# Kernel optimization log

Measured on AMD Instinct MI355X. Metric: run time of the kernel, lower is better.

## Reference

```python
import jax, jax.numpy as jnp
import numpy as np

N_HEAD, D_MODEL, DQ, DK, DV = 16, 1024, 64, 64, 64
B, LQ, LK = 2, 2048, 2048
EPS = 1e-3


def setup_inputs() -> dict:
    key = jax.random.key(0)
    ks = jax.random.split(key, 8)
    v = jax.random.normal(ks[0], (B, LK, D_MODEL), jnp.float32)
    k = jax.random.normal(ks[1], (B, LK, D_MODEL), jnp.float32)
    q = jax.random.normal(ks[2], (B, LQ, D_MODEL), jnp.float32)
    mask = jax.random.randint(ks[3], (B, LQ, LK), 0, 2).astype(bool)
    # xavier_normal for [n_head, d_model, d*]: fan_in=d_model, fan_out=d* (per torch, last two dims)
    def xav(kk, shape):
        std = np.sqrt(2.0 / (shape[-2] + shape[-1]))
        return jax.random.normal(kk, shape, jnp.float32) * std
    w_q = xav(ks[4], (N_HEAD, D_MODEL, DQ))
    w_k = xav(ks[5], (N_HEAD, D_MODEL, DK))
    w_v = xav(ks[6], (N_HEAD, D_MODEL, DV))
    # output linear: torch default init; use uniform(-1/sqrt(fan_in), ..)
    fan_in = N_HEAD * DV
    bound = 1.0 / np.sqrt(fan_in)
    kw, kb = jax.random.split(ks[7])
    w_o = jax.random.uniform(kw, (fan_in, D_MODEL), jnp.float32, -bound, bound)
    b_o = jax.random.uniform(kb, (D_MODEL,), jnp.float32, -bound, bound)
    gamma = jnp.ones((D_MODEL,), jnp.float32)
    beta = jnp.zeros((D_MODEL,), jnp.float32)
    return {"v": v, "k": k, "q": q, "mask": mask, "w_q": w_q, "w_k": w_k,
            "w_v": w_v, "w_o": w_o, "b_o": b_o, "gamma": gamma, "beta": beta}


def _layer_norm(x, gamma, beta):
    mean = jnp.mean(x, axis=-1, keepdims=True)
    # torch.std default is unbiased (ddof=1); eps added to std (not var)
    std = jnp.std(x, axis=-1, keepdims=True, ddof=1)
    return (x - mean) / (std + EPS) * gamma + beta


def reference(v, k, q, mask, w_q, w_k, w_v, w_o, b_o, gamma, beta):
    residual = k  # source uses k as residual
    # per-head projections: [h, b, l, d*]
    qh = jnp.einsum('bld,hde->hble', q, w_q)
    kh = jnp.einsum('bld,hde->hble', k, w_k)
    vh = jnp.einsum('bld,hde->hble', v, w_v)
    scale = 1.0 / np.sqrt(DK)
    scores = jnp.einsum('hbqe,hbke->hbqk', qh, kh) * scale  # [h,b,Lq,Lk]
    scores = jnp.where(mask[None], -jnp.inf, scores)
    attn = jax.nn.softmax(scores, axis=-1)
    out = jnp.einsum('hbqk,hbke->hbqe', attn, vh)  # [h,b,Lq,dv]
    # cat(split(out, batch, dim=0), dim=-1): heads concatenated on last dim
    out = out.transpose(1, 2, 0, 3).reshape(out.shape[1], out.shape[2], -1)
    out = out @ w_o + b_o
    x = out + residual  # dropout is identity in eval
    return _layer_norm(x, gamma, beta)
```

## Files before the change

### kernel.cpp

```cpp
#include <hip/hip_runtime.h>
#include <math.h>

typedef __bf16 bf16_t;
typedef bf16_t bf16x8 __attribute__((ext_vector_type(8)));
typedef float  f32x4  __attribute__((ext_vector_type(4)));
typedef unsigned short u16;
typedef u16 ushortx4 __attribute__((ext_vector_type(4)));
typedef unsigned long long u64;

#define MFMA16(a, b, c) __builtin_amdgcn_mfma_f32_16x16x32_bf16((a), (b), (c), 0, 0, 0)

__device__ __forceinline__ u16 f2bf(float f) {
    unsigned int u = __float_as_uint(f);
    u = (u + 0x7fffu + ((u >> 16) & 1u)) >> 16;
    return (u16)u;
}

__device__ __forceinline__ float bf2f(unsigned int u) {
    return __uint_as_float(u << 16);
}

__device__ __forceinline__ void gld16(const u16* g, u16* l) {
    __builtin_amdgcn_global_load_lds(
        (const __attribute__((address_space(1))) void*)g,
        (__attribute__((address_space(3))) void*)l, 16, 0, 0);
}


__global__ __launch_bounds__(256) void k_prep(const float* __restrict__ q,
                                              const float* __restrict__ k,
                                              const float* __restrict__ v,
                                              const int* __restrict__ mask,
                                              u16* __restrict__ qb,
                                              u16* __restrict__ kb,
                                              u16* __restrict__ vb,
                                              u64* __restrict__ mask64) {
    int bid = blockIdx.x;
    if (bid < 12288) {
        int sel = bid >> 12;
        int i = (bid & 4095) * 256 + threadIdx.x;
        const float* src = sel == 0 ? q : (sel == 1 ? k : v);
        u16* dst = sel == 0 ? qb : (sel == 1 ? kb : vb);
        float4 val = ((const float4*)src)[i];
        ushortx4 r;
        r[0] = f2bf(val.x); r[1] = f2bf(val.y); r[2] = f2bf(val.z); r[3] = f2bf(val.w);
        ((ushortx4*)dst)[i] = r;
    } else {
        int b2 = bid - 12288;
        int ktg = b2 & 7, q4 = (b2 >> 3) & 511, b = b2 >> 12;
        int wave = threadIdx.x >> 6, lane = threadIdx.x & 63;
        int qq = q4 * 4 + wave;
        const int* mp = mask + ((size_t)(b * 2048 + qq)) * 2048 + ktg * 256 + lane;
#pragma unroll
        for (int i = 0; i < 4; ++i) {
            int m = mp[i * 64];
            u64 bal = __ballot(m != 0);
            if (lane == 0) mask64[((size_t)(b * 32 + ktg * 4 + i)) * 2048 + qq] = bal;
        }
    }
}

__global__ __launch_bounds__(256) void k_prepw(const float* __restrict__ w_q,
                                               const float* __restrict__ w_k,
                                               const float* __restrict__ w_v,
                                               const float* __restrict__ w_o,
                                               u16* __restrict__ wqt,
                                               u16* __restrict__ wkt,
                                               u16* __restrict__ wvt,
                                               u16* __restrict__ wot) {
    __shared__ float tile[32][33];
    int bid = blockIdx.x;
    const float* src;
    u16* dst;
    int r0, c0, R, C;
    if (bid < 3072) {
        int x = bid & 31, y = (bid >> 5) & 1, z = bid >> 6;
        int h = z & 15, sel = z >> 4;
        src = (sel == 0 ? w_q : (sel == 1 ? w_k : w_v)) + (size_t)h * 65536;
        dst = (sel == 0 ? wqt : (sel == 1 ? wkt : wvt)) + (size_t)h * 65536;
        r0 = x * 32; c0 = y * 32; R = 1024; C = 64;
    } else {
        int t = bid - 3072;
        r0 = (t & 31) * 32; c0 = (t >> 5) * 32; R = 1024; C = 1024;
        src = w_o; dst = wot;
    }
    int tx = threadIdx.x & 31, ty = threadIdx.x >> 5;
    const float* s = src + ((size_t)r0) * C + c0;
#pragma unroll
    for (int i = 0; i < 4; ++i) tile[ty + i * 8][tx] = s[(ty + i * 8) * (size_t)C + tx];
    __syncthreads();
    u16* d = dst + ((size_t)c0) * R + r0;
#pragma unroll
    for (int i = 0; i < 4; ++i) d[(ty + i * 8) * (size_t)R + tx] = f2bf(tile[tx][ty + i * 8]);
}

#define GEMM_CORE(Ablk, Bblk, ACC)                                                    \
    int c0 = wave * 2;                                                                \
    const u16* Ag0 = Ablk + (size_t)(c0 * 16 + l15) * 1024 + quad * 8;                \
    const u16* Ag1 = Ablk + (size_t)((c0 + 1) * 16 + l15) * 1024 + quad * 8;          \
    const u16* Bg0 = Bblk + (size_t)(c0 * 16 + l15) * 1024 + quad * 8;                \
    const u16* Bg1 = Bblk + (size_t)((c0 + 1) * 16 + l15) * 1024 + quad * 8;          \
    gld16(Ag0, As + c0 * 512); gld16(Ag1, As + (c0 + 1) * 512);                       \
    gld16(Bg0, Bs + c0 * 512); gld16(Bg1, Bs + (c0 + 1) * 512);                       \
    __syncthreads();                                                                  \
    int buf = 0;                                                                      \
    for (int ks = 0; ks < 32; ++ks) {                                                 \
        if (ks < 31) {                                                                \
            int k0 = (ks + 1) * 32;                                                   \
            gld16(Ag0 + k0, As + (buf ^ 1) * 4096 + c0 * 512);                        \
            gld16(Ag1 + k0, As + (buf ^ 1) * 4096 + (c0 + 1) * 512);                  \
            gld16(Bg0 + k0, Bs + (buf ^ 1) * 4096 + c0 * 512);                        \
            gld16(Bg1 + k0, Bs + (buf ^ 1) * 4096 + (c0 + 1) * 512);                  \
        }                                                                             \
        bf16x8 af[4], bfr[4];                                                         \
        _Pragma("unroll")                                                             \
        for (int i = 0; i < 4; ++i)                                                   \
            af[i] = *(const bf16x8*)(As + buf * 4096 + (wy * 4 + i) * 512 + lane * 8);\
        _Pragma("unroll")                                                             \
        for (int j = 0; j < 4; ++j)                                                   \
            bfr[j] = *(const bf16x8*)(Bs + buf * 4096 + (wx * 4 + j) * 512 + lane * 8);\
        _Pragma("unroll")                                                             \
        for (int i = 0; i < 4; ++i)                                                   \
            _Pragma("unroll")                                                         \
            for (int j = 0; j < 4; ++j) ACC[i][j] = MFMA16(af[i], bfr[j], ACC[i][j]); \
        __syncthreads();                                                              \
        buf ^= 1;                                                                     \
    }

__global__ __launch_bounds__(256) void k_proj(
    const u16* __restrict__ qb, const u16* __restrict__ kb, const u16* __restrict__ vb,
    const u16* __restrict__ wqt, const u16* __restrict__ wkt, const u16* __restrict__ wvt,
    u16* __restrict__ oq, u16* __restrict__ okh, u16* __restrict__ ovt) {
    __shared__ __align__(16) u16 smem[18432];
    u16* As = smem;
    u16* Bs = smem + 8192;
    int z = blockIdx.y, gx = blockIdx.x;
    int bm, bn;
    const u16 *A, *B;
    if (z == 0)      { bm = gx >> 3; bn = gx & 7; A = qb; B = wqt; }
    else if (z == 1) { bm = gx >> 3; bn = gx & 7; A = kb; B = wkt; }
    else             { bm = gx & 7; bn = gx >> 3; A = wvt; B = vb; }
    A += (size_t)bm * 128 * 1024;
    B += (size_t)bn * 128 * 1024;
    int tid = threadIdx.x, wave = tid >> 6, lane = tid & 63;
    int wy = wave >> 1, wx = wave & 1, l15 = lane & 15, quad = lane >> 4;
    f32x4 acc[4][4] = {};
    GEMM_CORE(A, B, acc)
    u16* ep = smem + wave * 4608;
    float mulf = (z == 0) ? 0.18033688011112042f : 1.0f;
#pragma unroll
    for (int i = 0; i < 4; ++i)
#pragma unroll
        for (int j = 0; j < 4; ++j)
#pragma unroll
            for (int r = 0; r < 4; ++r)
                ep[(i * 16 + quad * 4 + r) * 72 + j * 16 + l15] = f2bf(acc[i][j][r] * mulf);
    int rl = lane >> 3, cg = lane & 7;
    if (z < 2) {
        int hh = bn * 2 + wx;
        int m0 = bm * 128 + wy * 64;
        int bb = m0 >> 11, l0 = m0 & 2047;
        u16* O = (z ? okh : oq) + ((size_t)((hh * 2 + bb) * 2048 + l0)) * 64;
#pragma unroll
        for (int s = 0; s < 8; ++s) {
            int row = s * 8 + rl;
            uint4 v = *(const uint4*)(ep + row * 72 + cg * 8);
            *(uint4*)(O + (size_t)row * 64 + cg * 8) = v;
        }
    } else {
        int m0 = bm * 128 + wy * 64;
        int hh = m0 >> 6;
        int n0 = bn * 128 + wx * 64;
        int bb = n0 >> 11, l0 = n0 & 2047;
        u16* O = ovt + (size_t)(hh * 2 + bb) * 131072 + (size_t)(m0 & 63) * 2048 + l0;
#pragma unroll
        for (int s = 0; s < 8; ++s) {
            int row = s * 8 + rl;
            uint4 v = *(const uint4*)(ep + row * 72 + cg * 8);
            *(uint4*)(O + (size_t)row * 2048 + cg * 8) = v;
        }
    }
}

__global__ __launch_bounds__(256) void k_attn(
    const u16* __restrict__ qh, const u16* __restrict__ kh,
    const u16* __restrict__ vt, const u64* __restrict__ mask64,
    u16* __restrict__ po, float* __restrict__ pl) {
    int qt = blockIdx.x, hb = blockIdx.y, ksp = blockIdx.z;
    int b = hb & 1;
    int tid = threadIdx.x, wave = tid >> 6, lane = tid & 63;
    int l15 = lane & 15, quad = lane >> 4;

    __shared__ __align__(16) u16 Ks[2][4096], Vs[2][4096];
    __shared__ __align__(16) u16 Pb[4][1024];

    int qrow0 = qt * 128 + wave * 32;
    const u16* Qp = qh + ((size_t)(hb * 2048) + qrow0 + l15) * 64 + quad * 8;
    bf16x8 qf[2][2];
    qf[0][0] = *(const bf16x8*)Qp;
    qf[0][1] = *(const bf16x8*)(Qp + 32);
    qf[1][0] = *(const bf16x8*)(Qp + 1024);
    qf[1][1] = *(const bf16x8*)(Qp + 1024 + 32);

    int c0 = wave * 2;
    const u16* Kg0 = kh + (size_t)hb * 131072 + (size_t)ksp * 65536 +
                     (size_t)(wave * 16 + l15) * 64 + quad * 8;
    const u16* Kg1 = Kg0 + 32;
    const u16* Vg0 = vt + (size_t)hb * 131072 + (size_t)(wave * 16 + l15) * 2048 +
                     ksp * 1024 + quad * 8;
    const u16* Vg1 = Vg0 + 32;
    const u64* Mp = mask64 + (size_t)b * 65536 + (size_t)ksp * 32768 + qrow0 + l15;

    float l_lane[2] = {0.f, 0.f};
    f32x4 o[2][4] = {};

    gld16(Kg0, &Ks[0][c0 * 512]);
    gld16(Kg1, &Ks[0][(c0 + 1) * 512]);
    gld16(Vg0, &Vs[0][c0 * 512]);
    gld16(Vg1, &Vs[0][(c0 + 1) * 512]);
    u64 mw0 = Mp[0], mw1 = Mp[16];
    __syncthreads();
    int buf = 0;
    int swz = (l15 & 7) << 3;
    for (int kt = 0; kt < 16; ++kt) {
        u64 mwn0 = 0, mwn1 = 0;
        if (kt < 15) {
            gld16(Kg0 + (size_t)(kt + 1) * 4096, &Ks[buf ^ 1][c0 * 512]);
            gld16(Kg1 + (size_t)(kt + 1) * 4096, &Ks[buf ^ 1][(c0 + 1) * 512]);
            gld16(Vg0 + (size_t)(kt + 1) * 64, &Vs[buf ^ 1][c0 * 512]);
            gld16(Vg1 + (size_t)(kt + 1) * 64, &Vs[buf ^ 1][(c0 + 1) * 512]);
            mwn0 = Mp[(size_t)(kt + 1) * 2048];
            mwn1 = Mp[(size_t)(kt + 1) * 2048 + 16];
        }
        bf16x8 kf[8], vf[8];
#pragma unroll
        for (int c = 0; c < 8; ++c) kf[c] = *(const bf16x8*)&Ks[buf][c * 512 + lane * 8];
#pragma unroll
        for (int c = 0; c < 8; ++c) vf[c] = *(const bf16x8*)&Vs[buf][c * 512 + lane * 8];
#pragma unroll
        for (int hf = 0; hf < 2; ++hf) {
            u64 mw = hf ? mw1 : mw0;
            f32x4 st[4] = {};
#pragma unroll
            for (int t = 0; t < 4; ++t) {
                st[t] = MFMA16(kf[t * 2], qf[hf][0], st[t]);
                st[t] = MFMA16(kf[t * 2 + 1], qf[hf][1], st[t]);
            }
            unsigned int w0 = (unsigned int)(mw >> (quad * 4));
            unsigned int w1 = (unsigned int)(mw >> (32 + quad * 4));
#pragma unroll
            for (int r = 0; r < 4; ++r) {
                st[0][r] = ((w0 >> r) & 1u) ? -3e30f : st[0][r];
                st[1][r] = ((w0 >> (16 + r)) & 1u) ? -3e30f : st[1][r];
                st[2][r] = ((w1 >> r) & 1u) ? -3e30f : st[2][r];
                st[3][r] = ((w1 >> (16 + r)) & 1u) ? -3e30f : st[3][r];
            }
            float ll = 0.f;
#pragma unroll
            for (int t = 0; t < 4; ++t) {
                float p0 = __builtin_amdgcn_exp2f(st[t][0]);
                float p1 = __builtin_amdgcn_exp2f(st[t][1]);
                float p2 = __builtin_amdgcn_exp2f(st[t][2]);
                float p3 = __builtin_amdgcn_exp2f(st[t][3]);
                ll += (p0 + p1) + (p2 + p3);
                uint2 pk;
                pk.x = (__float_as_uint(p1) & 0xffff0000u) | (__float_as_uint(p0) >> 16);
                pk.y = (__float_as_uint(p3) & 0xffff0000u) | (__float_as_uint(p2) >> 16);
                int g = t * 2 + (quad >> 1);
                int phys = l15 * 64 + (((g << 3) ^ swz)) + (quad & 1) * 4;
                *(uint2*)&Pb[wave][phys] = pk;
            }
            l_lane[hf] += ll;
#pragma unroll
            for (int kc = 0; kc < 2; ++kc) {
                int g = kc * 4 + quad;
                bf16x8 pf = *(const bf16x8*)&Pb[wave][l15 * 64 + (((g << 3) ^ swz))];
#pragma unroll
                for (int t = 0; t < 4; ++t)
                    o[hf][t] = MFMA16(pf, vf[t * 2 + kc], o[hf][t]);
            }
        }
        mw0 = mwn0; mw1 = mwn1;
        __syncthreads();
        buf ^= 1;
    }
    size_t rowbase = ((size_t)ksp * 32 + hb) * 2048 + qrow0;
    int rl = lane >> 3, cg = lane & 7;
#pragma unroll
    for (int hf = 0; hf < 2; ++hf) {
        float ls = l_lane[hf];
        ls += __shfl_xor(ls, 16, 64);
        ls += __shfl_xor(ls, 32, 64);
        if (quad == 0) pl[rowbase + hf * 16 + l15] = ls;
#pragma unroll
        for (int t = 0; t < 4; ++t)
#pragma unroll
            for (int r = 0; r < 4; ++r) {
                int row = quad * 4 + r, col = t * 16 + l15;
                int g = col >> 3;
                Pb[wave][row * 64 + (((g ^ (row & 7)) << 3)) + (col & 7)] =
                    f2bf(o[hf][t][r]);
            }
#pragma unroll
        for (int s = 0; s < 2; ++s) {
            int row = s * 8 + rl;
            uint4 v = *(const uint4*)&Pb[wave][row * 64 + ((cg ^ (row & 7)) << 3)];
            *(uint4*)(po + (rowbase + hf * 16 + row) * 64 + cg * 8) = v;
        }
    }
}

__global__ __launch_bounds__(256) void k_amerge(const u16* __restrict__ po,
                                                const float* __restrict__ pl,
                                                u16* __restrict__ ao) {
    int bid = blockIdx.x;
    int hb = bid >> 6, rc = bid & 63;
    int h = hb >> 1, b = hb & 1;
    int tid = threadIdx.x;
    int r = tid >> 3, c = tid & 7;
    int row = rc * 32 + r;
    size_t i0 = ((size_t)hb * 2048 + row) * 64 + c * 8;
    uint4 a0 = *(const uint4*)(po + i0);
    uint4 a1 = *(const uint4*)(po + i0 + 4194304);
    float l0 = pl[(size_t)hb * 2048 + row];
    float l1 = pl[65536 + (size_t)hb * 2048 + row];
    float inv = 1.0f / (l0 + l1);
    unsigned int* pa0 = (unsigned int*)&a0;
    unsigned int* pa1 = (unsigned int*)&a1;
    uint4 out;
    unsigned int* po_ = (unsigned int*)&out;
#pragma unroll
    for (int i = 0; i < 4; ++i) {
        float lo = (bf2f(pa0[i] & 0xffffu) + bf2f(pa1[i] & 0xffffu)) * inv;
        float hi = (bf2f(pa0[i] >> 16) + bf2f(pa1[i] >> 16)) * inv;
        po_[i] = (unsigned int)f2bf(lo) | ((unsigned int)f2bf(hi) << 16);
    }
    *(uint4*)(ao + ((size_t)(b * 2048 + row)) * 1024 + h * 64 + c * 8) = out;
}

__global__ __launch_bounds__(512) void k_out(
    const u16* __restrict__ ao, const u16* __restrict__ wot,
    float* __restrict__ xp0, float* __restrict__ xp1) {
    __shared__ __align__(16) u16 smem[18432];
    u16* As = smem;
    u16* Bs = smem + 8192;
    int gx = blockIdx.x, bm = gx >> 3, bn = gx & 7;
    int ksp = blockIdx.y;
    const u16* A = ao + (size_t)bm * 128 * 1024 + ksp * 512;
    const u16* B = wot + (size_t)bn * 128 * 1024 + ksp * 512;
    float* xp = ksp ? xp1 : xp0;
    int tid = threadIdx.x, wave = tid >> 6, lane = tid & 63;
    int wy = wave >> 2, wx = wave & 3, l15 = lane & 15, quad = lane >> 4;
    const u16* Ag = A + (size_t)(wave * 16 + l15) * 1024 + quad * 8;
    const u16* Bg = B + (size_t)(wave * 16 + l15) * 1024 + quad * 8;
    f32x4 acc[4][2] = {};
    gld16(Ag, As + wave * 512);
    gld16(Bg, Bs + wave * 512);
    __syncthreads();
    int buf = 0;
    for (int ks = 0; ks < 16; ++ks) {
        if (ks < 15) {
            int k0 = (ks + 1) * 32;
            gld16(Ag + k0, As + (buf ^ 1) * 4096 + wave * 512);
            gld16(Bg + k0, Bs + (buf ^ 1) * 4096 + wave * 512);
        }
        bf16x8 af[4], bfr[2];
#pragma unroll
        for (int i = 0; i < 4; ++i)
            af[i] = *(const bf16x8*)(As + buf * 4096 + (wy * 4 + i) * 512 + lane * 8);
#pragma unroll
        for (int j = 0; j < 2; ++j)
            bfr[j] = *(const bf16x8*)(Bs + buf * 4096 + (wx * 2 + j) * 512 + lane * 8);
#pragma unroll
        for (int i = 0; i < 4; ++i)
#pragma unroll
            for (int j = 0; j < 2; ++j) acc[i][j] = MFMA16(af[i], bfr[j], acc[i][j]);
        __syncthreads();
        buf ^= 1;
    }
    float* epf = (float*)smem + wave * 1152;
    int rl = lane >> 3, cg = lane & 7;
    int mbase = bm * 128 + wy * 64, nbase = bn * 128 + wx * 32;
#pragma unroll
    for (int cc = 0; cc < 2; ++cc) {
#pragma unroll
        for (int i2 = 0; i2 < 2; ++i2)
#pragma unroll
            for (int j = 0; j < 2; ++j)
#pragma unroll
                for (int r = 0; r < 4; ++r)
                    epf[(i2 * 16 + quad * 4 + r) * 36 + j * 16 + l15] =
                        acc[cc * 2 + i2][j][r];
#pragma unroll
        for (int s = 0; s < 4; ++s) {
            int row = s * 8 + rl;
            f32x4 v = *(const f32x4*)(epf + row * 36 + cg * 4);
            int m = mbase + cc * 32 + row, n = nbase + cg * 4;
            *(f32x4*)(xp + (size_t)m * 1024 + n) = v;
        }
    }
}

__global__ __launch_bounds__(256) void k_ln(const float* __restrict__ xp0,
                                            const float* __restrict__ xp1,
                                            const float* __restrict__ resid,
                                            const float* __restrict__ bo,
                                            const float* __restrict__ gamma,
                                            const float* __restrict__ beta,
                                            float* __restrict__ out) {
    int row = blockIdx.x;
    size_t base = (size_t)row * 256;
    float4 a0 = ((const float4*)xp0)[base + threadIdx.x];
    float4 a1 = ((const float4*)xp1)[base + threadIdx.x];
    float4 rs = ((const float4*)resid)[base + threadIdx.x];
    float4 b4 = ((const float4*)bo)[threadIdx.x];
    float4 v;
    v.x = a0.x + a1.x + rs.x + b4.x;
    v.y = a0.y + a1.y + rs.y + b4.y;
    v.z = a0.z + a1.z + rs.z + b4.z;
    v.w = a0.w + a1.w + rs.w + b4.w;
    float s = v.x + v.y + v.z + v.w;
    float ss = v.x * v.x + v.y * v.y + v.z * v.z + v.w * v.w;
#pragma unroll
    for (int off = 32; off; off >>= 1) {
        s += __shfl_down(s, off, 64);
        ss += __shfl_down(ss, off, 64);
    }
    __shared__ float sb[8];
    int wave = threadIdx.x >> 6, lane = threadIdx.x & 63;
    if (lane == 0) { sb[wave] = s; sb[4 + wave] = ss; }
    __syncthreads();
    s = sb[0] + sb[1] + sb[2] + sb[3];
    ss = sb[4] + sb[5] + sb[6] + sb[7];
    float mean = s * (1.0f / 1024.0f);
    float var = fmaxf((ss - 1024.0f * mean * mean) * (1.0f / 1023.0f), 0.f);
    float inv = 1.0f / (sqrtf(var) + 1e-3f);
    float4 g = ((const float4*)gamma)[threadIdx.x];
    float4 bt = ((const float4*)beta)[threadIdx.x];
    float4 o;
    o.x = (v.x - mean) * inv * g.x + bt.x;
    o.y = (v.y - mean) * inv * g.y + bt.y;
    o.z = (v.z - mean) * inv * g.z + bt.z;
    o.w = (v.w - mean) * inv * g.w + bt.w;
    ((float4*)(out))[base + threadIdx.x] = o;
}

extern "C" void kernel_launch(void* const* d_in, const int* in_sizes, int n_in,
                              void* d_out, int out_size, void* d_ws, size_t ws_size,
                              hipStream_t stream) {
    const float* v_in  = (const float*)d_in[0];
    const float* k_in  = (const float*)d_in[1];
    const float* q_in  = (const float*)d_in[2];
    const int*   mask  = (const int*)d_in[3];
    const float* w_q   = (const float*)d_in[4];
    const float* w_k   = (const float*)d_in[5];
    const float* w_v   = (const float*)d_in[6];
    const float* w_o   = (const float*)d_in[7];
    const float* b_o   = (const float*)d_in[8];
    const float* gamma = (const float*)d_in[9];
    const float* beta  = (const float*)d_in[10];
    float* out = (float*)d_out;

    char* ws = (char*)d_ws;
    const size_t MB = 1ull << 20;
    u16* qb  = (u16*)(ws + 0 * MB);
    u16* kb  = (u16*)(ws + 8 * MB);
    u16* vb  = (u16*)(ws + 16 * MB);
    u16* wqt = (u16*)(ws + 24 * MB);
    u16* wkt = (u16*)(ws + 26 * MB);
    u16* wvt = (u16*)(ws + 28 * MB);
    u16* wot = (u16*)(ws + 30 * MB);
    u16* qh  = (u16*)(ws + 32 * MB);
    u16* kh  = (u16*)(ws + 40 * MB);
    u16* vt  = (u16*)(ws + 48 * MB);
    u16* ao  = (u16*)(ws + 56 * MB);
    u64* mask64 = (u64*)(ws + 64 * MB);
    u16*   po = (u16*)(ws + 0 * MB);
    float* pl = (float*)(ws + 16 * MB);
    float* xp0 = (float*)(ws + 32 * MB);
    float* xp1 = (float*)(ws + 64 * MB);

    k_prep<<<dim3(20480), dim3(256), 0, stream>>>(q_in, k_in, v_in, mask,
                                                  qb, kb, vb, mask64);
    k_prepw<<<dim3(4096), dim3(256), 0, stream>>>(w_q, w_k, w_v, w_o,
                                                  wqt, wkt, wvt, wot);
    k_proj<<<dim3(256, 3), dim3(256), 0, stream>>>(qb, kb, vb, wqt, wkt, wvt, qh, kh, vt);
    k_attn<<<dim3(16, 32, 2), dim3(256), 0, stream>>>(qh, kh, vt, mask64, po, pl);
    k_amerge<<<dim3(2048), dim3(256), 0, stream>>>(po, pl, ao);
    k_out<<<dim3(256, 2), dim3(512), 0, stream>>>(ao, wot, xp0, xp1);
    k_ln<<<dim3(4096), dim3(256), 0, stream>>>(xp0, xp1, k_in, b_o, gamma, beta, out);
}
```

Measured before the change: 308.9 us.

## Merge weight prep into input prep kernel and reorder block indices for L2 reuse

Folds the weight transpose/convert kernel into the input conversion and mask-packing kernel, which removes one kernel launch. It also remaps block indices in the projection, attention and output GEMMs so that consecutive blocks share the same weight tile or the same query tile across heads. The aim is better L2 and MALL reuse of the shared operands. The merged kernel now declares a shared tile for every block, which may cost a little occupancy on the elementwise paths.

```diff
diff --git a/kernel.cpp b/kernel.cpp
--- a/kernel.cpp
+++ b/kernel.cpp
@@ -31,10 +31,19 @@
                                               const float* __restrict__ k,
                                               const float* __restrict__ v,
                                               const int* __restrict__ mask,
+                                              const float* __restrict__ w_q,
+                                              const float* __restrict__ w_k,
+                                              const float* __restrict__ w_v,
+                                              const float* __restrict__ w_o,
                                               u16* __restrict__ qb,
                                               u16* __restrict__ kb,
                                               u16* __restrict__ vb,
-                                              u64* __restrict__ mask64) {
+                                              u64* __restrict__ mask64,
+                                              u16* __restrict__ wqt,
+                                              u16* __restrict__ wkt,
+                                              u16* __restrict__ wvt,
+                                              u16* __restrict__ wot) {
+    __shared__ float tile[32][33];
     int bid = blockIdx.x;
     if (bid < 12288) {
         int sel = bid >> 12;
@@ -45,7 +54,7 @@
         ushortx4 r;
         r[0] = f2bf(val.x); r[1] = f2bf(val.y); r[2] = f2bf(val.z); r[3] = f2bf(val.w);
         ((ushortx4*)dst)[i] = r;
-    } else {
+    } else if (bid < 20480) {
         int b2 = bid - 12288;
         int ktg = b2 & 7, q4 = (b2 >> 3) & 511, b = b2 >> 12;
         int wave = threadIdx.x >> 6, lane = threadIdx.x & 63;
@@ -57,41 +66,31 @@
             u64 bal = __ballot(m != 0);
             if (lane == 0) mask64[((size_t)(b * 32 + ktg * 4 + i)) * 2048 + qq] = bal;
         }
-    }
-}
-
-__global__ __launch_bounds__(256) void k_prepw(const float* __restrict__ w_q,
-                                               const float* __restrict__ w_k,
-                                               const float* __restrict__ w_v,
-                                               const float* __restrict__ w_o,
-                                               u16* __restrict__ wqt,
-                                               u16* __restrict__ wkt,
-                                               u16* __restrict__ wvt,
-                                               u16* __restrict__ wot) {
-    __shared__ float tile[32][33];
-    int bid = blockIdx.x;
-    const float* src;
-    u16* dst;
-    int r0, c0, R, C;
-    if (bid < 3072) {
-        int x = bid & 31, y = (bid >> 5) & 1, z = bid >> 6;
-        int h = z & 15, sel = z >> 4;
-        src = (sel == 0 ? w_q : (sel == 1 ? w_k : w_v)) + (size_t)h * 65536;
-        dst = (sel == 0 ? wqt : (sel == 1 ? wkt : wvt)) + (size_t)h * 65536;
-        r0 = x * 32; c0 = y * 32; R = 1024; C = 64;
     } else {
-        int t = bid - 3072;
-        r0 = (t & 31) * 32; c0 = (t >> 5) * 32; R = 1024; C = 1024;
-        src = w_o; dst = wot;
-    }
-    int tx = threadIdx.x & 31, ty = threadIdx.x >> 5;
-    const float* s = src + ((size_t)r0) * C + c0;
-#pragma unroll
-    for (int i = 0; i < 4; ++i) tile[ty + i * 8][tx] = s[(ty + i * 8) * (size_t)C + tx];
-    __syncthreads();
-    u16* d = dst + ((size_t)c0) * R + r0;
-#pragma unroll
-    for (int i = 0; i < 4; ++i) d[(ty + i * 8) * (size_t)R + tx] = f2bf(tile[tx][ty + i * 8]);
+        int b3 = bid - 20480;
+        const float* src;
+        u16* dst;
+        int r0, c0, C;
+        if (b3 < 3072) {
+            int x = b3 & 31, y = (b3 >> 5) & 1, z = b3 >> 6;
+            int h = z & 15, sel = z >> 4;
+            src = (sel == 0 ? w_q : (sel == 1 ? w_k : w_v)) + (size_t)h * 65536;
+            dst = (sel == 0 ? wqt : (sel == 1 ? wkt : wvt)) + (size_t)h * 65536;
+            r0 = x * 32; c0 = y * 32; C = 64;
+        } else {
+            int t = b3 - 3072;
+            r0 = (t & 31) * 32; c0 = (t >> 5) * 32; C = 1024;
+            src = w_o; dst = wot;
+        }
+        int tx = threadIdx.x & 31, ty = threadIdx.x >> 5;
+        const float* s = src + ((size_t)r0) * C + c0;
+#pragma unroll
+        for (int i = 0; i < 4; ++i) tile[ty + i * 8][tx] = s[(ty + i * 8) * (size_t)C + tx];
+        __syncthreads();
+        u16* d = dst + ((size_t)c0) * 1024 + r0;
+#pragma unroll
+        for (int i = 0; i < 4; ++i) d[(ty + i * 8) * 1024 + tx] = f2bf(tile[tx][ty + i * 8]);
+    }
 }
 
 #define GEMM_CORE(Ablk, Bblk, ACC)                                                    \
@@ -137,9 +136,9 @@
     int z = blockIdx.y, gx = blockIdx.x;
     int bm, bn;
     const u16 *A, *B;
-    if (z == 0)      { bm = gx >> 3; bn = gx & 7; A = qb; B = wqt; }
-    else if (z == 1) { bm = gx >> 3; bn = gx & 7; A = kb; B = wkt; }
-    else             { bm = gx & 7; bn = gx >> 3; A = wvt; B = vb; }
+    if (z == 0)      { bm = gx & 31; bn = gx >> 5; A = qb; B = wqt; }
+    else if (z == 1) { bm = gx & 31; bn = gx >> 5; A = kb; B = wkt; }
+    else             { bn = gx & 31; bm = gx >> 5; A = wvt; B = vb; }
     A += (size_t)bm * 128 * 1024;
     B += (size_t)bn * 128 * 1024;
     int tid = threadIdx.x, wave = tid >> 6, lane = tid & 63;
@@ -186,7 +185,7 @@
     const u16* __restrict__ qh, const u16* __restrict__ kh,
     const u16* __restrict__ vt, const u64* __restrict__ mask64,
     u16* __restrict__ po, float* __restrict__ pl) {
-    int qt = blockIdx.x, hb = blockIdx.y, ksp = blockIdx.z;
+    int hb = blockIdx.x, qt = blockIdx.y, ksp = blockIdx.z;
     int b = hb & 1;
     int tid = threadIdx.x, wave = tid >> 6, lane = tid & 63;
     int l15 = lane & 15, quad = lane >> 4;
@@ -344,7 +343,7 @@
     __shared__ __align__(16) u16 smem[18432];
     u16* As = smem;
     u16* Bs = smem + 8192;
-    int gx = blockIdx.x, bm = gx >> 3, bn = gx & 7;
+    int gx = blockIdx.x, bm = gx & 31, bn = gx >> 5;
     int ksp = blockIdx.y;
     const u16* A = ao + (size_t)bm * 128 * 1024 + ksp * 512;
     const u16* B = wot + (size_t)bn * 128 * 1024 + ksp * 512;
@@ -480,12 +479,12 @@
     float* xp0 = (float*)(ws + 32 * MB);
     float* xp1 = (float*)(ws + 64 * MB);
 
-    k_prep<<<dim3(20480), dim3(256), 0, stream>>>(q_in, k_in, v_in, mask,
-                                                  qb, kb, vb, mask64);
-    k_prepw<<<dim3(4096), dim3(256), 0, stream>>>(w_q, w_k, w_v, w_o,
+    k_prep<<<dim3(24576), dim3(256), 0, stream>>>(q_in, k_in, v_in, mask,
+                                                  w_q, w_k, w_v, w_o,
+                                                  qb, kb, vb, mask64,
                                                   wqt, wkt, wvt, wot);
     k_proj<<<dim3(256, 3), dim3(256), 0, stream>>>(qb, kb, vb, wqt, wkt, wvt, qh, kh, vt);
-    k_attn<<<dim3(16, 32, 2), dim3(256), 0, stream>>>(qh, kh, vt, mask64, po, pl);
+    k_attn<<<dim3(32, 16, 2), dim3(256), 0, stream>>>(qh, kh, vt, mask64, po, pl);
     k_amerge<<<dim3(2048), dim3(256), 0, stream>>>(po, pl, ao);
     k_out<<<dim3(256, 2), dim3(512), 0, stream>>>(ao, wot, xp0, xp1);
     k_ln<<<dim3(4096), dim3(256), 0, stream>>>(xp0, xp1, k_in, b_o, gamma, beta, out);
```

Result: faster. 301.0 us (-2.5%).
